# Performance work log

Hardware: AMD Instinct MI355X
Metric: run time of the kernel (lower is better)

## Reference

```python
import jax, jax.numpy as jnp
import numpy as np

M, IN_F, OUT_F = 16384, 2048, 2048

def sign_fn(x):
    # torch.sign(torch.sign(x) + 0.5): maps 0 -> +1, otherwise +/-1
    return jnp.sign(jnp.sign(x) + 0.5)

def setup_inputs() -> dict:
    key = jax.random.key(0)
    kx, kw = jax.random.split(key)
    # Upstream BNN activations are binary +/-1 (required for the packed-bit
    # backward in the original module to be exact).
    x = sign_fn(jax.random.normal(kx, (M, IN_F), dtype=jnp.float32))
    weight = jax.random.uniform(kw, (OUT_F, IN_F), dtype=jnp.float32) * 0.01
    return {"x": x, "weight": weight}

def reference(x, weight):
    # xnor=False path: SignFunctionNoSTE -> binarize weight, then dense matmul
    b_weight = sign_fn(weight)          # [OUT_F, IN_F], values in {-1, +1}
    return x @ b_weight.T               # [M, OUT_F]
```

## Files before the change

### kernel.cpp

```cpp
#include <hip/hip_runtime.h>
#include <stdint.h>

typedef unsigned long long u64;

#define M_DIM 16384
#define N_DIM 2048
#define K_DIM 2048

#define BM 128
#define BN 256
#define BK 64
#define NSTAGE (K_DIM / BK)

typedef int v4i  __attribute__((ext_vector_type(4)));
typedef int v16i __attribute__((ext_vector_type(16)));


__device__ __forceinline__ int pk4(float a, float b, float c, float d) {
    int r = (a < 0.0f ? 0xFF : 0x01);
    r |= (b < 0.0f ? 0xFF : 0x01) << 8;
    r |= (c < 0.0f ? 0xFF : 0x01) << 16;
    r |= (d < 0.0f ? 0xFF : 0x01) << 24;
    return r;
}

template <int T>
__global__ __launch_bounds__(256) void pack_i8_kernel(
        const float* __restrict__ src, char* __restrict__ dst) {
    const int wave_id = (blockIdx.x * 256 + threadIdx.x) >> 6;
    const int lane = threadIdx.x & 63;
    const int s  = wave_id & (NSTAGE - 1);
    const int rg = wave_id >> 5;
    const int r  = lane & 31;
    const int kh = lane >> 5;
    const int regs = 2 * T;
    char* out = dst + ((size_t)rg * NSTAGE + s) * (regs * 1024) + lane * 16;
#pragma unroll 2
    for (int rr = 0; rr < regs; ++rr) {
        const int c = rr / T, t = rr % T;
        const int row = rg * (T * 32) + t * 32 + r;
        const float* p = src + (size_t)row * K_DIM + s * BK + c * 32 + kh * 16;
        const float4 v0 = ((const float4*)p)[0];
        const float4 v1 = ((const float4*)p)[1];
        const float4 v2 = ((const float4*)p)[2];
        const float4 v3 = ((const float4*)p)[3];
        int4 o;
        o.x = pk4(v0.x, v0.y, v0.z, v0.w);
        o.y = pk4(v1.x, v1.y, v1.z, v1.w);
        o.z = pk4(v2.x, v2.y, v2.z, v2.w);
        o.w = pk4(v3.x, v3.y, v3.z, v3.w);
        *(int4*)(out + rr * 1024) = o;
    }
}

struct Frags {
    v4i a[2][2];
    v4i b[2][4];
};

__device__ __forceinline__ void load_frags(
        Frags& f, const char* __restrict__ aS, const char* __restrict__ bS,
        int wm, int wn) {
#pragma unroll
    for (int c = 0; c < 2; ++c) {
#pragma unroll
        for (int i = 0; i < 2; ++i)
            f.a[c][i] = *(const v4i*)(aS + (c * 4 + wm + i) * 1024);
#pragma unroll
        for (int j = 0; j < 4; ++j)
            f.b[c][j] = *(const v4i*)(bS + (c * 8 + wn + j) * 1024);
    }
}

__global__ __launch_bounds__(256, 2) void bgemm_i8_kernel(
        const char* __restrict__ Ap, const char* __restrict__ Bp,
        float* __restrict__ C) {
    const int t    = threadIdx.x;
    const int lane = t & 63;
    const int wv   = t >> 6;

    const int id    = blockIdx.x;
    const int xcd   = id & 7;
    const int idx   = id >> 3;
    const int m_blk = xcd * 16 + (idx & 15);
    const int n_blk = idx >> 4;

    const int wm = (wv >> 1) * 2;
    const int wn = (wv & 1) * 4;

    const char* aS = Ap + (size_t)m_blk * (NSTAGE * 8192)  + lane * 16;
    const char* bS = Bp + (size_t)n_blk * (NSTAGE * 16384) + lane * 16;

    v16i acc[2][4];
#pragma unroll
    for (int i = 0; i < 2; ++i)
#pragma unroll
        for (int j = 0; j < 4; ++j)
#pragma unroll
            for (int q = 0; q < 16; ++q) acc[i][j][q] = 0;

    auto compute = [&](const Frags& f) {
#pragma unroll
        for (int c = 0; c < 2; ++c)
#pragma unroll
            for (int i = 0; i < 2; ++i)
#pragma unroll
                for (int j = 0; j < 4; ++j)
                    acc[i][j] = __builtin_amdgcn_mfma_i32_32x32x32_i8(
                        f.a[c][i], f.b[c][j], acc[i][j], 0, 0, 0);
    };

    Frags f0, f1;
    load_frags(f0, aS, bS, wm, wn);
#pragma unroll 1
    for (int s = 0; s < NSTAGE; s += 2) {
        load_frags(f1, aS + (size_t)(s + 1) * 8192,
                        bS + (size_t)(s + 1) * 16384, wm, wn);
        compute(f0);
        if (s + 2 < NSTAGE)
            load_frags(f0, aS + (size_t)(s + 2) * 8192,
                            bS + (size_t)(s + 2) * 16384, wm, wn);
        compute(f1);
    }

    const int col = lane & 31;
    const int rq  = (lane >> 5) * 4;
#pragma unroll
    for (int i = 0; i < 2; ++i) {
#pragma unroll
        for (int j = 0; j < 4; ++j) {
            const int mbase = m_blk * BM + (wm + i) * 32;
            const int nbase = n_blk * BN + (wn + j) * 32;
#pragma unroll
            for (int q = 0; q < 16; ++q) {
                const int row = mbase + (q & 3) + 8 * (q >> 2) + rq;
                C[(size_t)row * N_DIM + nbase + col] = (float)acc[i][j][q];
            }
        }
    }
}

#define KC 32
#define KT 16
struct alignas(16) u64x2 { u64 x, y; };

__global__ __launch_bounds__(256) void pack_sign_kernel(
        const float* __restrict__ in, u64* __restrict__ out, int ngroups) {
    int wid  = (blockIdx.x * 256 + threadIdx.x) >> 6;
    int lane = threadIdx.x & 63;
    if (wid >= ngroups) return;
    const float4* p = reinterpret_cast<const float4*>(in) + (size_t)wid * 64 + lane;
    float4 v = *p;
    u64 b0 = __ballot(v.x < 0.0f);
    u64 b1 = __ballot(v.y < 0.0f);
    u64 b2 = __ballot(v.z < 0.0f);
    u64 b3 = __ballot(v.w < 0.0f);
    if (lane == 0) {
        u64* o = out + (size_t)wid * 4;
        o[0] = b0; o[1] = b1; o[2] = b2; o[3] = b3;
    }
}

__global__ __launch_bounds__(256, 2) void bgemm_kernel(
        const u64* __restrict__ A, const u64* __restrict__ B,
        float* __restrict__ C) {
    __shared__ u64 As[KT][128];
    __shared__ u64 Bs[KT][128];
    const int t     = threadIdx.x;
    const int m_blk = blockIdx.y << 7;
    const int n_blk = blockIdx.x << 7;
    const int lane = t & 63;
    const int wave = t >> 6;
    const int tm   = lane >> 3;
    const int tn   = lane & 7;
    const int m0   = ((wave >> 1) << 6) + (tm << 3);
    const int n0   = ((wave & 1) << 6) + (tn << 3);
    unsigned acc[8][8];
#pragma unroll
    for (int i = 0; i < 8; ++i)
#pragma unroll
        for (int j = 0; j < 8; ++j) acc[i][j] = 0u;
    const int sr = t >> 3;
    const int sc = (t << 1) & 15;
    for (int ks = 0; ks < K_DIM / (KT * 64); ++ks) {
        const int cbase = ks * KT;
#pragma unroll
        for (int i = 0; i < 4; ++i) {
            int r = i * 32 + sr;
            u64x2 va = *reinterpret_cast<const u64x2*>(A + (size_t)(m_blk + r) * KC + cbase + sc);
            As[sc][r] = va.x; As[sc + 1][r] = va.y;
            u64x2 vb = *reinterpret_cast<const u64x2*>(B + (size_t)(n_blk + r) * KC + cbase + sc);
            Bs[sc][r] = vb.x; Bs[sc + 1][r] = vb.y;
        }
        __syncthreads();
#pragma unroll 1
        for (int c = 0; c < KT; ++c) {
            u64 a[8], b[8];
#pragma unroll
            for (int i = 0; i < 4; ++i) {
                u64x2 va = *reinterpret_cast<const u64x2*>(&As[c][m0 + 2 * i]);
                a[2 * i] = va.x; a[2 * i + 1] = va.y;
                u64x2 vb = *reinterpret_cast<const u64x2*>(&Bs[c][n0 + 2 * i]);
                b[2 * i] = vb.x; b[2 * i + 1] = vb.y;
            }
#pragma unroll
            for (int i = 0; i < 8; ++i)
#pragma unroll
                for (int j = 0; j < 8; ++j)
                    acc[i][j] += (unsigned)__builtin_popcountll(a[i] ^ b[j]);
        }
        __syncthreads();
    }
#pragma unroll
    for (int i = 0; i < 8; ++i) {
        float* o = C + (size_t)(m_blk + m0 + i) * N_DIM + n_blk + n0;
        float4 v0, v1;
        v0.x = (float)(K_DIM - 2 * (int)acc[i][0]);
        v0.y = (float)(K_DIM - 2 * (int)acc[i][1]);
        v0.z = (float)(K_DIM - 2 * (int)acc[i][2]);
        v0.w = (float)(K_DIM - 2 * (int)acc[i][3]);
        v1.x = (float)(K_DIM - 2 * (int)acc[i][4]);
        v1.y = (float)(K_DIM - 2 * (int)acc[i][5]);
        v1.z = (float)(K_DIM - 2 * (int)acc[i][6]);
        v1.w = (float)(K_DIM - 2 * (int)acc[i][7]);
        *reinterpret_cast<float4*>(o)     = v0;
        *reinterpret_cast<float4*>(o + 4) = v1;
    }
}

extern "C" void kernel_launch(void* const* d_in, const int* in_sizes, int n_in,
                              void* d_out, int out_size, void* d_ws, size_t ws_size,
                              hipStream_t stream) {
    const float* x = (const float*)d_in[0];
    const float* w = (const float*)d_in[1];
    float* out = (float*)d_out;

    const size_t needA = (size_t)M_DIM * K_DIM;
    const size_t needB = (size_t)N_DIM * K_DIM;
    if (ws_size >= needA + needB) {
        char* Ap = (char*)d_ws;
        char* Bp = Ap + needA;
        pack_i8_kernel<4><<<4096 / 4, 256, 0, stream>>>(x, Ap);
        pack_i8_kernel<8><<<256 / 4, 256, 0, stream>>>(w, Bp);
        bgemm_i8_kernel<<<(M_DIM / BM) * (N_DIM / BN), 256, 0, stream>>>(Ap, Bp, out);
    } else {
        u64* xb = (u64*)d_ws;
        u64* wb = xb + (size_t)M_DIM * KC;
        int xgroups = (M_DIM * K_DIM) / 256;
        int wgroups = (N_DIM * K_DIM) / 256;
        pack_sign_kernel<<<xgroups / 4, 256, 0, stream>>>(x, xb, xgroups);
        pack_sign_kernel<<<wgroups / 4, 256, 0, stream>>>(w, wb, wgroups);
        bgemm_kernel<<<dim3(N_DIM / 128, M_DIM / 128), 256, 0, stream>>>(xb, wb, out);
    }
}
```

Before: 338.9 us.

## Enlarge int8 GEMM tile to 256x256 and stage A via global_load_lds

Doubles the M tile to 256 so each wave computes a 128x128 sub-tile with 16 accumulators. The A operand is now copied straight into LDS with global_load_lds, double-buffered per wave, while B fragments still go to registers. The block-to-tile mapping and the A packing layout are changed to match. The aim is more reuse per loaded byte and less global load traffic per MFMA, at the cost of occupancy dropping to one block per CU and a higher register count.

```diff
diff --git a/kernel.cpp b/kernel.cpp
--- a/kernel.cpp
+++ b/kernel.cpp
@@ -7,7 +7,7 @@
 #define N_DIM 2048
 #define K_DIM 2048
 
-#define BM 128
+#define BM 256
 #define BN 256
 #define BK 64
 #define NSTAGE (K_DIM / BK)
@@ -15,6 +15,13 @@
 typedef int v4i  __attribute__((ext_vector_type(4)));
 typedef int v16i __attribute__((ext_vector_type(16)));
 
+
+__device__ __forceinline__ void gld16(void* lds_base, const void* gsrc) {
+    __builtin_amdgcn_global_load_lds(
+        (const __attribute__((address_space(1))) uint32_t*)gsrc,
+        (__attribute__((address_space(3))) uint32_t*)lds_base,
+        16, 0, 0);
+}
 
 __device__ __forceinline__ int pk4(float a, float b, float c, float d) {
     int r = (a < 0.0f ? 0xFF : 0x01);
@@ -53,84 +60,87 @@
     }
 }
 
-struct Frags {
-    v4i a[2][2];
-    v4i b[2][4];
-};
-
-__device__ __forceinline__ void load_frags(
-        Frags& f, const char* __restrict__ aS, const char* __restrict__ bS,
-        int wm, int wn) {
-#pragma unroll
-    for (int c = 0; c < 2; ++c) {
-#pragma unroll
-        for (int i = 0; i < 2; ++i)
-            f.a[c][i] = *(const v4i*)(aS + (c * 4 + wm + i) * 1024);
-#pragma unroll
-        for (int j = 0; j < 4; ++j)
-            f.b[c][j] = *(const v4i*)(bS + (c * 8 + wn + j) * 1024);
-    }
-}
-
-__global__ __launch_bounds__(256, 2) void bgemm_i8_kernel(
+__global__ __launch_bounds__(256, 1) void bgemm_i8_kernel(
         const char* __restrict__ Ap, const char* __restrict__ Bp,
         float* __restrict__ C) {
+    __shared__ __align__(16) char lds[4][2][8192];
+
     const int t    = threadIdx.x;
     const int lane = t & 63;
     const int wv   = t >> 6;
+    const int hm   = wv >> 1;
+    const int hn   = wv & 1;
 
     const int id    = blockIdx.x;
     const int xcd   = id & 7;
-    const int idx   = id >> 3;
-    const int m_blk = xcd * 16 + (idx & 15);
-    const int n_blk = idx >> 4;
-
-    const int wm = (wv >> 1) * 2;
-    const int wn = (wv & 1) * 4;
-
-    const char* aS = Ap + (size_t)m_blk * (NSTAGE * 8192)  + lane * 16;
-    const char* bS = Bp + (size_t)n_blk * (NSTAGE * 16384) + lane * 16;
-
-    v16i acc[2][4];
-#pragma unroll
-    for (int i = 0; i < 2; ++i)
+    const int g     = id >> 3;
+    const int kk    = g & 31;
+    const int round = g >> 5;
+    const int m_blk = xcd * 8 + (kk >> 2);
+    const int n_blk = round * 4 + (kk & 3);
+
+    const char* aG = Ap + (size_t)m_blk * (NSTAGE * 16384) + lane * 16;
+    const char* bG = Bp + (size_t)n_blk * (NSTAGE * 16384) + lane * 16;
+
+    v16i acc[4][4];
+#pragma unroll
+    for (int i = 0; i < 4; ++i)
 #pragma unroll
         for (int j = 0; j < 4; ++j)
 #pragma unroll
             for (int q = 0; q < 16; ++q) acc[i][j][q] = 0;
 
-    auto compute = [&](const Frags& f) {
+    auto dmaA = [&](int s, int buf) {
+        const char* a = aG + (size_t)s * 16384;
+#pragma unroll
+        for (int r = 0; r < 8; ++r) {
+            const int reg = (r >> 2) * 8 + hm * 4 + (r & 3);
+            gld16(&lds[wv][buf][r * 1024], a + reg * 1024);
+        }
+    };
+    auto loadB = [&](int s, v4i bf[2][4]) {
+        const char* b = bG + (size_t)s * 16384;
 #pragma unroll
         for (int c = 0; c < 2; ++c)
 #pragma unroll
-            for (int i = 0; i < 2; ++i)
+            for (int j = 0; j < 4; ++j)
+                bf[c][j] = *(const v4i*)(b + (c * 8 + hn * 4 + j) * 1024);
+    };
+    auto compute = [&](int buf, v4i bf[2][4]) {
+#pragma unroll
+        for (int c = 0; c < 2; ++c) {
+            v4i af[4];
+#pragma unroll
+            for (int i = 0; i < 4; ++i)
+                af[i] = *(const v4i*)(&lds[wv][buf][(c * 4 + i) * 1024] + lane * 16);
+#pragma unroll
+            for (int i = 0; i < 4; ++i)
 #pragma unroll
                 for (int j = 0; j < 4; ++j)
                     acc[i][j] = __builtin_amdgcn_mfma_i32_32x32x32_i8(
-                        f.a[c][i], f.b[c][j], acc[i][j], 0, 0, 0);
+                        af[i], bf[c][j], acc[i][j], 0, 0, 0);
+        }
     };
 
-    Frags f0, f1;
-    load_frags(f0, aS, bS, wm, wn);
+    v4i bf0[2][4], bf1[2][4];
+    dmaA(0, 0); loadB(0, bf0);
+    dmaA(1, 1); loadB(1, bf1);
 #pragma unroll 1
     for (int s = 0; s < NSTAGE; s += 2) {
-        load_frags(f1, aS + (size_t)(s + 1) * 8192,
-                        bS + (size_t)(s + 1) * 16384, wm, wn);
-        compute(f0);
-        if (s + 2 < NSTAGE)
-            load_frags(f0, aS + (size_t)(s + 2) * 8192,
-                            bS + (size_t)(s + 2) * 16384, wm, wn);
-        compute(f1);
+        compute(0, bf0);
+        if (s + 2 < NSTAGE) { dmaA(s + 2, 0); loadB(s + 2, bf0); }
+        compute(1, bf1);
+        if (s + 3 < NSTAGE) { dmaA(s + 3, 1); loadB(s + 3, bf1); }
     }
 
     const int col = lane & 31;
     const int rq  = (lane >> 5) * 4;
 #pragma unroll
-    for (int i = 0; i < 2; ++i) {
+    for (int i = 0; i < 4; ++i) {
 #pragma unroll
         for (int j = 0; j < 4; ++j) {
-            const int mbase = m_blk * BM + (wm + i) * 32;
-            const int nbase = n_blk * BN + (wn + j) * 32;
+            const int mbase = m_blk * BM + (hm * 4 + i) * 32;
+            const int nbase = n_blk * BN + (hn * 4 + j) * 32;
 #pragma unroll
             for (int q = 0; q < 16; ++q) {
                 const int row = mbase + (q & 3) + 8 * (q >> 2) + rq;
@@ -240,7 +250,7 @@
     if (ws_size >= needA + needB) {
         char* Ap = (char*)d_ws;
         char* Bp = Ap + needA;
-        pack_i8_kernel<4><<<4096 / 4, 256, 0, stream>>>(x, Ap);
+        pack_i8_kernel<8><<<2048 / 4, 256, 0, stream>>>(x, Ap);
         pack_i8_kernel<8><<<256 / 4, 256, 0, stream>>>(w, Bp);
         bgemm_i8_kernel<<<(M_DIM / BM) * (N_DIM / BN), 256, 0, stream>>>(Ap, Bp, out);
     } else {
```

After: 480.3 us. +41.7%, slower.
